# Kernel tuning notes

Hardware: AMD Instinct MI355X
Metric: run time of the kernel (lower is better)

Reference implementation:

```python
import jax, jax.numpy as jnp
import numpy as np

BATCH = 8192
NUM_VECTORS = 512
LATENT_DIM = 64


def setup_inputs() -> dict:
    key = jax.random.key(0)
    k1, k2 = jax.random.split(key)
    x = jax.random.normal(k1, (BATCH, LATENT_DIM), dtype=jnp.float32)
    # glorot_uniform init for the codebook
    limit = np.sqrt(6.0 / (NUM_VECTORS + LATENT_DIM)).astype(np.float32)
    trainable_p = jax.random.uniform(
        k2, (NUM_VECTORS, LATENT_DIM), dtype=jnp.float32,
        minval=-limit, maxval=limit)
    return {"x": x, "trainable_p": trainable_p}


def reference(x, trainable_p):
    # distances: (batch, num_vectors) Euclidean cdist
    diff = x[:, None, :] - trainable_p[None, :, :]   # (B, V, D)
    distances = jnp.sqrt(jnp.sum(jnp.square(diff), axis=-1))
    # r1: min over batch for each codebook vector, then mean over codebook
    r1_cost = jnp.mean(jnp.min(distances, axis=0), axis=-1)
    # r2: min over codebook for each sample, then mean over batch
    r2_cost = jnp.mean(jnp.min(distances, axis=-1), axis=-1)
    return distances, r1_cost, r2_cost
```

## Files before the change

kernel.cpp:

```cpp
#include <hip/hip_runtime.h>

#define BATCH 8192
#define NV 512
#define LD 64
#define RPB 16


__global__ __launch_bounds__(256) void setup_kernel(const float* __restrict__ x,
                                                    unsigned* __restrict__ r1bits,
                                                    float* __restrict__ r2sum,
                                                    float* __restrict__ xnorm) {
  int tid = blockIdx.x * blockDim.x + threadIdx.x;
  if (tid < NV) r1bits[tid] = 0x7f800000u;
  if (tid == 0) *r2sum = 0.f;
  if (tid < BATCH) {
    const float4* xr = (const float4*)(x + tid * LD);
    float acc = 0.f;
#pragma unroll
    for (int i = 0; i < LD / 4; ++i) {
      float4 v = xr[i];
      acc = fmaf(v.x, v.x, acc);
      acc = fmaf(v.y, v.y, acc);
      acc = fmaf(v.z, v.z, acc);
      acc = fmaf(v.w, v.w, acc);
    }
    xnorm[tid] = acc;
  }
}

__global__ __launch_bounds__(512) void dist_kernel(const float* __restrict__ x,
                                                   const float* __restrict__ p,
                                                   const float* __restrict__ xnorm,
                                                   float* __restrict__ out,
                                                   unsigned* __restrict__ r1bits,
                                                   float* __restrict__ r2sum) {
  const int v = threadIdx.x;
  const int r0 = blockIdx.x * RPB;
  const int wave = v >> 6, lane = v & 63;
  __shared__ float wmin[RPB][8];

  float4 pv[LD / 4];
  const float4* pr = (const float4*)(p + v * LD);
#pragma unroll
  for (int i = 0; i < LD / 4; ++i) pv[i] = pr[i];

  float pn = 0.f;
#pragma unroll
  for (int i = 0; i < LD / 4; ++i) {
    pn = fmaf(pv[i].x, pv[i].x, pn);
    pn = fmaf(pv[i].y, pv[i].y, pn);
    pn = fmaf(pv[i].z, pv[i].z, pn);
    pn = fmaf(pv[i].w, pv[i].w, pn);
  }

  float vmin = 3.4e38f;

  for (int r = 0; r < RPB; ++r) {
    const int row = r0 + r;
    const float* xr = x + row * LD;
    float a0 = 0.f, a1 = 0.f, a2 = 0.f, a3 = 0.f;
#pragma unroll
    for (int i = 0; i < LD / 4; ++i) {
      a0 = fmaf(xr[4 * i + 0], pv[i].x, a0);
      a1 = fmaf(xr[4 * i + 1], pv[i].y, a1);
      a2 = fmaf(xr[4 * i + 2], pv[i].z, a2);
      a3 = fmaf(xr[4 * i + 3], pv[i].w, a3);
    }
    float dot = (a0 + a1) + (a2 + a3);
    float d2 = xnorm[row] + pn - 2.f * dot;
    float dist = sqrtf(fmaxf(d2, 0.f));
    out[(long)row * NV + v] = dist;
    vmin = fminf(vmin, dist);

    float m = dist;
#pragma unroll
    for (int o = 32; o; o >>= 1) m = fminf(m, __shfl_xor(m, o));
    if (lane == 0) wmin[r][wave] = m;
  }

  atomicMin(&r1bits[v], __float_as_uint(vmin));

  __syncthreads();
  if (wave == 0) {
    float rm = 0.f;
    if (lane < RPB) {
      rm = wmin[lane][0];
#pragma unroll
      for (int w = 1; w < 8; ++w) rm = fminf(rm, wmin[lane][w]);
    }
#pragma unroll
    for (int o = 32; o; o >>= 1) rm += __shfl_xor(rm, o);
    if (lane == 0) atomicAdd(r2sum, rm);
  }
}

__global__ __launch_bounds__(512) void finalize_kernel(const unsigned* __restrict__ r1bits,
                                                       const float* __restrict__ r2sum,
                                                       float* __restrict__ out) {
  int tid = threadIdx.x;
  float val = __uint_as_float(r1bits[tid]);
#pragma unroll
  for (int o = 32; o; o >>= 1) val += __shfl_xor(val, o);
  __shared__ float ws[8];
  if ((tid & 63) == 0) ws[tid >> 6] = val;
  __syncthreads();
  if (tid == 0) {
    float s = 0.f;
    for (int w = 0; w < 8; ++w) s += ws[w];
    out[(long)BATCH * NV] = s / (float)NV;
    out[(long)BATCH * NV + 1] = r2sum[0] / (float)BATCH;
  }
}

extern "C" void kernel_launch(void* const* d_in, const int* in_sizes, int n_in,
                              void* d_out, int out_size, void* d_ws, size_t ws_size,
                              hipStream_t stream) {
  const float* x = (const float*)d_in[0];
  const float* p = (const float*)d_in[1];
  float* out = (float*)d_out;
  unsigned* r1bits = (unsigned*)d_ws;
  float* r2sum = (float*)d_ws + 512;
  float* xnorm = (float*)d_ws + 1024;

  hipLaunchKernelGGL(setup_kernel, dim3(BATCH / 256), dim3(256), 0, stream,
                     x, r1bits, r2sum, xnorm);
  hipLaunchKernelGGL(dist_kernel, dim3(BATCH / RPB), dim3(512), 0, stream,
                     x, p, xnorm, out, r1bits, r2sum);
  hipLaunchKernelGGL(finalize_kernel, dim3(1), dim3(512), 0, stream,
                     r1bits, r2sum, out);
}
```

Baseline: 89.65 us.

## Compute distance dot products with bf16 MFMA instead of scalar FMA loops

Replaces the per-thread scalar fp32 dot-product loop with 16x16x32 bf16 MFMA instructions. Each wave computes a 16-row by 64-column tile, converting x and codebook rows to bf16 on load. Codebook norms are now precomputed in the setup kernel, and row/column minima are reduced through shared memory before the atomics. The bf16 rounding of the dot product lowers distance accuracy, which can matter where the norm-expansion subtraction cancels.

Measured after the change: 87.01 us. 1.03x faster.

```diff
diff --git a/kernel.cpp b/kernel.cpp
--- a/kernel.cpp
+++ b/kernel.cpp
@@ -3,13 +3,32 @@
 #define BATCH 8192
 #define NV 512
 #define LD 64
-#define RPB 16
+
+typedef __attribute__((ext_vector_type(8))) short bf16x8;
+typedef __attribute__((ext_vector_type(4))) float f32x4;
 
 
+static __device__ __forceinline__ short f2bf(float f) {
+  unsigned u = __float_as_uint(f);
+  u += 0x7fff + ((u >> 16) & 1);
+  return (short)(u >> 16);
+}
+
+static __device__ __forceinline__ bf16x8 load8_bf16(const float* ptr) {
+  float4 f0 = *(const float4*)(ptr);
+  float4 f1 = *(const float4*)(ptr + 4);
+  bf16x8 r;
+  r[0] = f2bf(f0.x); r[1] = f2bf(f0.y); r[2] = f2bf(f0.z); r[3] = f2bf(f0.w);
+  r[4] = f2bf(f1.x); r[5] = f2bf(f1.y); r[6] = f2bf(f1.z); r[7] = f2bf(f1.w);
+  return r;
+}
+
 __global__ __launch_bounds__(256) void setup_kernel(const float* __restrict__ x,
+                                                    const float* __restrict__ p,
                                                     unsigned* __restrict__ r1bits,
                                                     float* __restrict__ r2sum,
-                                                    float* __restrict__ xnorm) {
+                                                    float* __restrict__ xnorm,
+                                                    float* __restrict__ pnorm) {
   int tid = blockIdx.x * blockDim.x + threadIdx.x;
   if (tid < NV) r1bits[tid] = 0x7f800000u;
   if (tid == 0) *r2sum = 0.f;
@@ -19,78 +38,114 @@
 #pragma unroll
     for (int i = 0; i < LD / 4; ++i) {
       float4 v = xr[i];
-      acc = fmaf(v.x, v.x, acc);
-      acc = fmaf(v.y, v.y, acc);
-      acc = fmaf(v.z, v.z, acc);
-      acc = fmaf(v.w, v.w, acc);
+      acc = fmaf(v.x, v.x, acc); acc = fmaf(v.y, v.y, acc);
+      acc = fmaf(v.z, v.z, acc); acc = fmaf(v.w, v.w, acc);
     }
     xnorm[tid] = acc;
+  }
+  if (tid < NV) {
+    const float4* pr = (const float4*)(p + tid * LD);
+    float acc = 0.f;
+#pragma unroll
+    for (int i = 0; i < LD / 4; ++i) {
+      float4 v = pr[i];
+      acc = fmaf(v.x, v.x, acc); acc = fmaf(v.y, v.y, acc);
+      acc = fmaf(v.z, v.z, acc); acc = fmaf(v.w, v.w, acc);
+    }
+    pnorm[tid] = acc;
   }
 }
 
 __global__ __launch_bounds__(512) void dist_kernel(const float* __restrict__ x,
                                                    const float* __restrict__ p,
-                                                   const float* __restrict__ xnorm,
+                                                   const float* __restrict__ xn,
+                                                   const float* __restrict__ pn,
                                                    float* __restrict__ out,
                                                    unsigned* __restrict__ r1bits,
                                                    float* __restrict__ r2sum) {
-  const int v = threadIdx.x;
-  const int r0 = blockIdx.x * RPB;
-  const int wave = v >> 6, lane = v & 63;
-  __shared__ float wmin[RPB][8];
+  const int tid = threadIdx.x;
+  const int w = tid >> 6;
+  const int lane = tid & 63;
+  const int lhi = lane >> 4;
+  const int llo = lane & 15;
+  const int r0 = blockIdx.x << 4;
+  const int colbase = w * 64;
 
-  float4 pv[LD / 4];
-  const float4* pr = (const float4*)(p + v * LD);
-#pragma unroll
-  for (int i = 0; i < LD / 4; ++i) pv[i] = pr[i];
+  __shared__ float r1buf[NV];
+  __shared__ float r2buf[8][16];
 
-  float pn = 0.f;
-#pragma unroll
-  for (int i = 0; i < LD / 4; ++i) {
-    pn = fmaf(pv[i].x, pv[i].x, pn);
-    pn = fmaf(pv[i].y, pv[i].y, pn);
-    pn = fmaf(pv[i].z, pv[i].z, pn);
-    pn = fmaf(pv[i].w, pv[i].w, pn);
+  const float* arow = x + (r0 + llo) * LD;
+  bf16x8 a0 = load8_bf16(arow + lhi * 8);
+  bf16x8 a1 = load8_bf16(arow + 32 + lhi * 8);
+
+  f32x4 acc0 = {0.f, 0.f, 0.f, 0.f}, acc1 = acc0, acc2 = acc0, acc3 = acc0;
+  {
+    const float* prow0 = p + (colbase + 0 * 16 + llo) * LD;
+    acc0 = __builtin_amdgcn_mfma_f32_16x16x32_bf16(a0, load8_bf16(prow0 + lhi * 8), acc0, 0, 0, 0);
+    acc0 = __builtin_amdgcn_mfma_f32_16x16x32_bf16(a1, load8_bf16(prow0 + 32 + lhi * 8), acc0, 0, 0, 0);
+    const float* prow1 = p + (colbase + 1 * 16 + llo) * LD;
+    acc1 = __builtin_amdgcn_mfma_f32_16x16x32_bf16(a0, load8_bf16(prow1 + lhi * 8), acc1, 0, 0, 0);
+    acc1 = __builtin_amdgcn_mfma_f32_16x16x32_bf16(a1, load8_bf16(prow1 + 32 + lhi * 8), acc1, 0, 0, 0);
+    const float* prow2 = p + (colbase + 2 * 16 + llo) * LD;
+    acc2 = __builtin_amdgcn_mfma_f32_16x16x32_bf16(a0, load8_bf16(prow2 + lhi * 8), acc2, 0, 0, 0);
+    acc2 = __builtin_amdgcn_mfma_f32_16x16x32_bf16(a1, load8_bf16(prow2 + 32 + lhi * 8), acc2, 0, 0, 0);
+    const float* prow3 = p + (colbase + 3 * 16 + llo) * LD;
+    acc3 = __builtin_amdgcn_mfma_f32_16x16x32_bf16(a0, load8_bf16(prow3 + lhi * 8), acc3, 0, 0, 0);
+    acc3 = __builtin_amdgcn_mfma_f32_16x16x32_bf16(a1, load8_bf16(prow3 + 32 + lhi * 8), acc3, 0, 0, 0);
   }
 
-  float vmin = 3.4e38f;
+  float xnr[4];
+#pragma unroll
+  for (int r = 0; r < 4; ++r) xnr[r] = xn[r0 + lhi * 4 + r];
 
-  for (int r = 0; r < RPB; ++r) {
-    const int row = r0 + r;
-    const float* xr = x + row * LD;
-    float a0 = 0.f, a1 = 0.f, a2 = 0.f, a3 = 0.f;
+  float rmin[4] = {3.4e38f, 3.4e38f, 3.4e38f, 3.4e38f};
+  float cmin[4];
 #pragma unroll
-    for (int i = 0; i < LD / 4; ++i) {
-      a0 = fmaf(xr[4 * i + 0], pv[i].x, a0);
-      a1 = fmaf(xr[4 * i + 1], pv[i].y, a1);
-      a2 = fmaf(xr[4 * i + 2], pv[i].z, a2);
-      a3 = fmaf(xr[4 * i + 3], pv[i].w, a3);
+  for (int t = 0; t < 4; ++t) {
+    const int col = colbase + t * 16 + llo;
+    const float pnc = pn[col];
+    const f32x4 a = (t == 0) ? acc0 : (t == 1) ? acc1 : (t == 2) ? acc2 : acc3;
+    float cm = 3.4e38f;
+#pragma unroll
+    for (int r = 0; r < 4; ++r) {
+      float d2 = xnr[r] + pnc - 2.f * a[r];
+      float dist = sqrtf(fmaxf(d2, 0.f));
+      out[(long)(r0 + lhi * 4 + r) * NV + col] = dist;
+      cm = fminf(cm, dist);
+      rmin[r] = fminf(rmin[r], dist);
     }
-    float dot = (a0 + a1) + (a2 + a3);
-    float d2 = xnorm[row] + pn - 2.f * dot;
-    float dist = sqrtf(fmaxf(d2, 0.f));
-    out[(long)row * NV + v] = dist;
-    vmin = fminf(vmin, dist);
-
-    float m = dist;
-#pragma unroll
-    for (int o = 32; o; o >>= 1) m = fminf(m, __shfl_xor(m, o));
-    if (lane == 0) wmin[r][wave] = m;
+    cmin[t] = cm;
   }
 
-  atomicMin(&r1bits[v], __float_as_uint(vmin));
+#pragma unroll
+  for (int t = 0; t < 4; ++t) {
+    float v = cmin[t];
+    v = fminf(v, __shfl_xor(v, 16));
+    v = fminf(v, __shfl_xor(v, 32));
+    if (lane < 16) r1buf[colbase + t * 16 + lane] = v;
+  }
+#pragma unroll
+  for (int r = 0; r < 4; ++r) {
+    float v = rmin[r];
+    v = fminf(v, __shfl_xor(v, 1));
+    v = fminf(v, __shfl_xor(v, 2));
+    v = fminf(v, __shfl_xor(v, 4));
+    v = fminf(v, __shfl_xor(v, 8));
+    if (llo == 0) r2buf[w][lhi * 4 + r] = v;
+  }
+  __syncthreads();
 
-  __syncthreads();
-  if (wave == 0) {
-    float rm = 0.f;
-    if (lane < RPB) {
-      rm = wmin[lane][0];
+  atomicMin(&r1bits[tid], __float_as_uint(r1buf[tid]));
+
+  if (tid < 16) {
+    float v = r2buf[0][tid];
 #pragma unroll
-      for (int w = 1; w < 8; ++w) rm = fminf(rm, wmin[lane][w]);
-    }
-#pragma unroll
-    for (int o = 32; o; o >>= 1) rm += __shfl_xor(rm, o);
-    if (lane == 0) atomicAdd(r2sum, rm);
+    for (int ww = 1; ww < 8; ++ww) v = fminf(v, r2buf[ww][tid]);
+    v += __shfl_xor(v, 1);
+    v += __shfl_xor(v, 2);
+    v += __shfl_xor(v, 4);
+    v += __shfl_xor(v, 8);
+    if (tid == 0) atomicAdd(r2sum, v);
   }
 }
 
@@ -121,11 +176,12 @@
   unsigned* r1bits = (unsigned*)d_ws;
   float* r2sum = (float*)d_ws + 512;
   float* xnorm = (float*)d_ws + 1024;
+  float* pnorm = (float*)d_ws + 9216;
 
   hipLaunchKernelGGL(setup_kernel, dim3(BATCH / 256), dim3(256), 0, stream,
-                     x, r1bits, r2sum, xnorm);
-  hipLaunchKernelGGL(dist_kernel, dim3(BATCH / RPB), dim3(512), 0, stream,
-                     x, p, xnorm, out, r1bits, r2sum);
+                     x, p, r1bits, r2sum, xnorm, pnorm);
+  hipLaunchKernelGGL(dist_kernel, dim3(BATCH / 16), dim3(512), 0, stream,
+                     x, p, xnorm, pnorm, out, r1bits, r2sum);
   hipLaunchKernelGGL(finalize_kernel, dim3(1), dim3(512), 0, stream,
                      r1bits, r2sum, out);
 }
```
